# Performance work log

Measured on AMD Instinct MI355X. Metric: run time of the kernel, lower is better.

Reference implementation:

```python
import jax, jax.numpy as jnp
import numpy as np

NUM_NODES = 5000
NUM_COLORS = 20
NODE_FEAT = 4
COLOR_FEAT = 3
COMBINED = NODE_FEAT + COLOR_FEAT  # 7
HIDDEN = 128
N_GRAPH = NUM_NODES * NUM_COLORS   # 100000 GCN nodes (batch=1)
N_EDGES = 1_600_000


def setup_inputs() -> dict:
    key = jax.random.key(0)
    ks = jax.random.split(key, 12)
    flat_obs = jax.random.normal(ks[0], (1, 3 + NUM_NODES * NODE_FEAT + NUM_COLORS * COLOR_FEAT), dtype=jnp.float32)
    edge_index = jax.random.randint(ks[1], (2, N_EDGES), 0, N_GRAPH, dtype=jnp.int64)
    s = lambda k, sh, fan: jax.random.normal(k, sh, dtype=jnp.float32) / np.sqrt(fan)
    return {
        "flat_obs": flat_obs,
        "edge_index": edge_index,
        "W1": s(ks[2], (COMBINED, HIDDEN), COMBINED),
        "b1": jnp.zeros((HIDDEN,), jnp.float32),
        "W2": s(ks[3], (HIDDEN, HIDDEN), HIDDEN),
        "b2": jnp.zeros((HIDDEN,), jnp.float32),
        "fc1_w": s(ks[4], (HIDDEN, HIDDEN), HIDDEN),
        "fc1_b": jnp.zeros((HIDDEN,), jnp.float32),
        "fc2_w": s(ks[5], (HIDDEN, 1), HIDDEN),
        "fc2_b": jnp.zeros((1,), jnp.float32),
    }


def _gcn_conv(x, W, b, src, dst, norm):
    # PyG GCNConv: out[dst] += norm * (x @ W)[src]; self-loops already in src/dst.
    xw = x @ W                                   # [N, H]
    msg = xw[src] * norm[:, None]                # [E+N, H]
    out = jax.ops.segment_sum(msg, dst, num_segments=N_GRAPH)
    return out + b


def reference(flat_obs, edge_index, W1, b1, W2, b2, fc1_w, fc1_b, fc2_w, fc2_b):
    B = flat_obs.shape[0]
    nf_start = 3
    nf_end = nf_start + NUM_NODES * NODE_FEAT
    cf_end = nf_end + NUM_COLORS * COLOR_FEAT
    node_features = flat_obs[:, nf_start:nf_end].reshape(B, NUM_NODES, NODE_FEAT)
    color_features = flat_obs[:, nf_end:cf_end].reshape(B, NUM_COLORS, COLOR_FEAT)

    # cross-expand: [B, nodes, colors, 4+3]
    en = jnp.broadcast_to(node_features[:, :, None, :], (B, NUM_NODES, NUM_COLORS, NODE_FEAT))
    ec = jnp.broadcast_to(color_features[:, None, :, :], (B, NUM_NODES, NUM_COLORS, COLOR_FEAT))
    combined = jnp.concatenate([en, ec], axis=3).reshape(-1, COMBINED)  # [N_GRAPH, 7]

    # add self loops + symmetric normalization (GCN)
    loops = jnp.arange(N_GRAPH, dtype=edge_index.dtype)
    src = jnp.concatenate([edge_index[0], loops])
    dst = jnp.concatenate([edge_index[1], loops])
    deg = jax.ops.segment_sum(jnp.ones_like(dst, dtype=jnp.float32), dst, num_segments=N_GRAPH)
    dinv = jnp.where(deg > 0, jax.lax.rsqrt(deg), 0.0)
    norm = dinv[src] * dinv[dst]

    x = jax.nn.relu(_gcn_conv(combined, W1, b1, src, dst, norm))
    x = jax.nn.relu(_gcn_conv(x, W2, b2, src, dst, norm))
    x = jax.nn.relu(x @ fc1_w + fc1_b)
    q = x @ fc2_w + fc2_b                         # [N_GRAPH, 1]
    return q.reshape(B, NUM_NODES * NUM_COLORS)
```

## Files before the change

kernel.cpp:

```cpp
#include <hip/hip_runtime.h>
#include <hip/hip_fp16.h>

#define NGRAPH 100000
#define NEDGE  1600000
#define HID    128
#define SCAN_B 512
#define NBLK   ((NGRAPH + SCAN_B - 1) / SCAN_B)
#define TILE   64

__device__ __forceinline__ int e_src(const int* ei, int is64, int e) {
    return is64 ? ei[2 * e] : ei[e];
}
__device__ __forceinline__ int e_dst(const int* ei, int is64, int e) {
    return is64 ? ei[2 * NEDGE + 2 * e] : ei[NEDGE + e];
}

__global__ void k_prep(const float* __restrict__ obs, const int* __restrict__ ei,
                       float* __restrict__ comb, int* __restrict__ deg,
                       int* __restrict__ fill, int* __restrict__ flag) {
    if (blockIdx.x == 0 && threadIdx.x < 64) {
        int v = ei[2 * threadIdx.x + 1];
        unsigned long long b = __ballot(v != 0);
        if (threadIdx.x == 0) flag[0] = (b == 0ull) ? 1 : 0;
    }
    int i = blockIdx.x * blockDim.x + threadIdx.x;
    if (i >= NGRAPH) return;
    int n = i / 20, c = i % 20;
    const float* nf = obs + 3 + n * 4;
    const float* cf = obs + 3 + 20000 + c * 3;
    float* o = comb + i * 7;
    o[0] = nf[0]; o[1] = nf[1]; o[2] = nf[2]; o[3] = nf[3];
    o[4] = cf[0]; o[5] = cf[1]; o[6] = cf[2];
    deg[i] = 0;
    fill[i] = 0;
}

__global__ void k_deg(const int* __restrict__ ei, const int* __restrict__ flag,
                      int* __restrict__ deg) {
    int e = blockIdx.x * blockDim.x + threadIdx.x;
    if (e >= NEDGE) return;
    atomicAdd(&deg[e_dst(ei, flag[0], e)], 1);
}

__global__ void __launch_bounds__(SCAN_B) k_scan1(const int* __restrict__ deg,
                                                  int* __restrict__ rowptr,
                                                  int* __restrict__ sums,
                                                  float* __restrict__ dinv) {
    __shared__ int sh[SCAN_B];
    int t = threadIdx.x;
    int i = blockIdx.x * SCAN_B + t;
    int val = (i < NGRAPH) ? deg[i] : 0;
    if (i < NGRAPH) dinv[i] = rsqrtf((float)(val + 1));
    sh[t] = val;
    __syncthreads();
    for (int o = 1; o < SCAN_B; o <<= 1) {
        int x = (t >= o) ? sh[t - o] : 0;
        __syncthreads();
        sh[t] += x;
        __syncthreads();
    }
    if (i < NGRAPH) rowptr[i] = sh[t] - val;
    if (t == SCAN_B - 1) sums[blockIdx.x] = sh[t];
}

__global__ void __launch_bounds__(256) k_scan2(int* __restrict__ sums) {
    __shared__ int sh[256];
    int t = threadIdx.x;
    int val = (t < NBLK) ? sums[t] : 0;
    sh[t] = val;
    __syncthreads();
    for (int o = 1; o < 256; o <<= 1) {
        int x = (t >= o) ? sh[t - o] : 0;
        __syncthreads();
        sh[t] += x;
        __syncthreads();
    }
    if (t < NBLK) sums[t] = sh[t] - val;
}

__global__ void __launch_bounds__(SCAN_B) k_scan3(int* __restrict__ rowptr,
                                                  const int* __restrict__ sums) {
    int i = blockIdx.x * SCAN_B + threadIdx.x;
    if (i < NGRAPH) rowptr[i] += sums[blockIdx.x];
}

__global__ void k_fill(const int* __restrict__ ei, const int* __restrict__ flag,
                       const float* __restrict__ dinv,
                       const int* __restrict__ rowptr, int* __restrict__ fill,
                       int2* __restrict__ csr) {
    int e = blockIdx.x * blockDim.x + threadIdx.x;
    if (e >= NEDGE) return;
    int is64 = flag[0];
    int s = e_src(ei, is64, e);
    int d = e_dst(ei, is64, e);
    int pos = rowptr[d] + atomicAdd(&fill[d], 1);
    csr[pos] = make_int2(s, __float_as_int(dinv[s] * dinv[d]));
}

__global__ void __launch_bounds__(256) k_gcn1(const int* __restrict__ rowptr,
                                              const int* __restrict__ deg,
                                              const int2* __restrict__ csr,
                                              const float* __restrict__ dinv,
                                              const float* __restrict__ comb,
                                              const float* __restrict__ W1,
                                              const float* __restrict__ b1,
                                              __half* __restrict__ x1) {
    __shared__ float agg_s[32][8];
    int g = threadIdx.x >> 3;
    int f = threadIdx.x & 7;
    int d = blockIdx.x * 32 + g;
    if (f < 7) {
        int start = rowptr[d], n = deg[d];
        float acc = 0.0f;
        for (int j = 0; j < n; ++j) {
            int2 ed = csr[start + j];
            acc += __int_as_float(ed.y) * comb[ed.x * 7 + f];
        }
        float dv = dinv[d];
        acc += dv * dv * comb[d * 7 + f];
        agg_s[g][f] = acc;
    }
    __syncthreads();
    float a[7];
    #pragma unroll
    for (int q = 0; q < 7; ++q) a[q] = agg_s[g][q];
    int h0 = f * 16;
    #pragma unroll
    for (int j = 0; j < 4; ++j) {
        int h = h0 + j * 4;
        float4 acc4 = *reinterpret_cast<const float4*>(b1 + h);
        #pragma unroll
        for (int q = 0; q < 7; ++q) {
            float4 w = *reinterpret_cast<const float4*>(W1 + q * HID + h);
            acc4.x = fmaf(a[q], w.x, acc4.x);
            acc4.y = fmaf(a[q], w.y, acc4.y);
            acc4.z = fmaf(a[q], w.z, acc4.z);
            acc4.w = fmaf(a[q], w.w, acc4.w);
        }
        __half2 h01 = __floats2half2_rn(fmaxf(acc4.x, 0.0f), fmaxf(acc4.y, 0.0f));
        __half2 h23 = __floats2half2_rn(fmaxf(acc4.z, 0.0f), fmaxf(acc4.w, 0.0f));
        uint2 pk;
        pk.x = *reinterpret_cast<unsigned int*>(&h01);
        pk.y = *reinterpret_cast<unsigned int*>(&h23);
        *reinterpret_cast<uint2*>(x1 + (size_t)d * HID + h) = pk;
    }
}

__global__ void __launch_bounds__(256) k_agg2(const int* __restrict__ rowptr,
                                              const int* __restrict__ deg,
                                              const int2* __restrict__ csr,
                                              const float* __restrict__ dinv,
                                              const __half2* __restrict__ x1,
                                              float* __restrict__ agg2) {
    int wave = threadIdx.x >> 6;
    int lane = threadIdx.x & 63;
    int d = blockIdx.x * 4 + wave;
    int f0 = lane * 2;
    int start = rowptr[d], n = deg[d];
    float2 acc = {0.0f, 0.0f};
    int j = 0;
    for (; j + 2 <= n; j += 2) {
        int2 e0 = csr[start + j];
        int2 e1 = csr[start + j + 1];
        float w0 = __int_as_float(e0.y);
        float w1 = __int_as_float(e1.y);
        float2 v0 = __half22float2(x1[(size_t)e0.x * 64 + lane]);
        float2 v1 = __half22float2(x1[(size_t)e1.x * 64 + lane]);
        acc.x = fmaf(w0, v0.x, acc.x);
        acc.y = fmaf(w0, v0.y, acc.y);
        acc.x = fmaf(w1, v1.x, acc.x);
        acc.y = fmaf(w1, v1.y, acc.y);
    }
    if (j < n) {
        int2 e0 = csr[start + j];
        float w0 = __int_as_float(e0.y);
        float2 v0 = __half22float2(x1[(size_t)e0.x * 64 + lane]);
        acc.x = fmaf(w0, v0.x, acc.x);
        acc.y = fmaf(w0, v0.y, acc.y);
    }
    float dv = dinv[d];
    float ws = dv * dv;
    float2 v = __half22float2(x1[(size_t)d * 64 + lane]);
    acc.x = fmaf(ws, v.x, acc.x);
    acc.y = fmaf(ws, v.y, acc.y);
    *reinterpret_cast<float2*>(agg2 + (size_t)d * HID + f0) = acc;
}

__device__ __forceinline__ void fmad(float4& acc, float s, const float4 w) {
    acc.x = fmaf(s, w.x, acc.x);
    acc.y = fmaf(s, w.y, acc.y);
    acc.z = fmaf(s, w.z, acc.z);
    acc.w = fmaf(s, w.w, acc.w);
}
__device__ __forceinline__ float4 relu4(float4 v) {
    float4 r;
    r.x = fmaxf(v.x, 0.0f); r.y = fmaxf(v.y, 0.0f);
    r.z = fmaxf(v.z, 0.0f); r.w = fmaxf(v.w, 0.0f);
    return r;
}

__global__ void __launch_bounds__(256, 3) k_mlp(const float* __restrict__ agg2,
                                                const float* __restrict__ W2,
                                                const float* __restrict__ b2,
                                                const float* __restrict__ fc1w,
                                                const float* __restrict__ fc1b,
                                                const float* __restrict__ fc2w,
                                                const float* __restrict__ fc2b,
                                                float* __restrict__ out) {
    __shared__ float as_[TILE][HID + 4];
    __shared__ float ws[32][HID + 4];
    const int tid = threadIdx.x;
    const int tx = tid & 15;
    const int ty = tid >> 4;
    const int n0 = blockIdx.x * TILE;
    const int hA = tx * 4;
    const int hB = 64 + tx * 4;

    #pragma unroll
    for (int q = 0; q < 8; ++q) {
        int idx = (q * 256 + tid) * 4;
        int row = idx >> 7, col = idx & 127;
        int nr = n0 + row; if (nr >= NGRAPH) nr = NGRAPH - 1;
        *reinterpret_cast<float4*>(&as_[row][col]) =
            *reinterpret_cast<const float4*>(agg2 + (size_t)nr * HID + col);
    }

    float4 cA[4], cB[4];
    {
        float4 bA = *reinterpret_cast<const float4*>(b2 + hA);
        float4 bB = *reinterpret_cast<const float4*>(b2 + hB);
        #pragma unroll
        for (int r = 0; r < 4; ++r) { cA[r] = bA; cB[r] = bB; }
    }
    for (int ks = 0; ks < HID; ks += 32) {
        #pragma unroll
        for (int q = 0; q < 4; ++q) {
            int idx = (q * 256 + tid) * 4;
            int row = idx >> 7, col = idx & 127;
            *reinterpret_cast<float4*>(&ws[row][col]) =
                *reinterpret_cast<const float4*>(W2 + (size_t)(ks + row) * HID + col);
        }
        __syncthreads();
        #pragma unroll
        for (int k = 0; k < 32; k += 4) {
            float4 wA0 = *reinterpret_cast<const float4*>(&ws[k + 0][hA]);
            float4 wB0 = *reinterpret_cast<const float4*>(&ws[k + 0][hB]);
            float4 wA1 = *reinterpret_cast<const float4*>(&ws[k + 1][hA]);
            float4 wB1 = *reinterpret_cast<const float4*>(&ws[k + 1][hB]);
            float4 wA2 = *reinterpret_cast<const float4*>(&ws[k + 2][hA]);
            float4 wB2 = *reinterpret_cast<const float4*>(&ws[k + 2][hB]);
            float4 wA3 = *reinterpret_cast<const float4*>(&ws[k + 3][hA]);
            float4 wB3 = *reinterpret_cast<const float4*>(&ws[k + 3][hB]);
            #pragma unroll
            for (int r = 0; r < 4; ++r) {
                float4 a = *reinterpret_cast<const float4*>(&as_[ty * 4 + r][ks + k]);
                fmad(cA[r], a.x, wA0); fmad(cB[r], a.x, wB0);
                fmad(cA[r], a.y, wA1); fmad(cB[r], a.y, wB1);
                fmad(cA[r], a.z, wA2); fmad(cB[r], a.z, wB2);
                fmad(cA[r], a.w, wA3); fmad(cB[r], a.w, wB3);
            }
        }
        __syncthreads();
    }
    #pragma unroll
    for (int r = 0; r < 4; ++r) {
        *reinterpret_cast<float4*>(&as_[ty * 4 + r][hA]) = relu4(cA[r]);
        *reinterpret_cast<float4*>(&as_[ty * 4 + r][hB]) = relu4(cB[r]);
    }

    float4 dA[4], dB[4];
    {
        float4 bA = *reinterpret_cast<const float4*>(fc1b + hA);
        float4 bB = *reinterpret_cast<const float4*>(fc1b + hB);
        #pragma unroll
        for (int r = 0; r < 4; ++r) { dA[r] = bA; dB[r] = bB; }
    }
    for (int ks = 0; ks < HID; ks += 32) {
        #pragma unroll
        for (int q = 0; q < 4; ++q) {
            int idx = (q * 256 + tid) * 4;
            int row = idx >> 7, col = idx & 127;
            *reinterpret_cast<float4*>(&ws[row][col]) =
                *reinterpret_cast<const float4*>(fc1w + (size_t)(ks + row) * HID + col);
        }
        __syncthreads();
        #pragma unroll
        for (int k = 0; k < 32; k += 4) {
            float4 wA0 = *reinterpret_cast<const float4*>(&ws[k + 0][hA]);
            float4 wB0 = *reinterpret_cast<const float4*>(&ws[k + 0][hB]);
            float4 wA1 = *reinterpret_cast<const float4*>(&ws[k + 1][hA]);
            float4 wB1 = *reinterpret_cast<const float4*>(&ws[k + 1][hB]);
            float4 wA2 = *reinterpret_cast<const float4*>(&ws[k + 2][hA]);
            float4 wB2 = *reinterpret_cast<const float4*>(&ws[k + 2][hB]);
            float4 wA3 = *reinterpret_cast<const float4*>(&ws[k + 3][hA]);
            float4 wB3 = *reinterpret_cast<const float4*>(&ws[k + 3][hB]);
            #pragma unroll
            for (int r = 0; r < 4; ++r) {
                float4 a = *reinterpret_cast<const float4*>(&as_[ty * 4 + r][ks + k]);
                fmad(dA[r], a.x, wA0); fmad(dB[r], a.x, wB0);
                fmad(dA[r], a.y, wA1); fmad(dB[r], a.y, wB1);
                fmad(dA[r], a.z, wA2); fmad(dB[r], a.z, wB2);
                fmad(dA[r], a.w, wA3); fmad(dB[r], a.w, wB3);
            }
        }
        __syncthreads();
    }

    float4 wqA = *reinterpret_cast<const float4*>(fc2w + hA);
    float4 wqB = *reinterpret_cast<const float4*>(fc2w + hB);
    float p[4];
    #pragma unroll
    for (int r = 0; r < 4; ++r) {
        float4 rA = relu4(dA[r]);
        float4 rB = relu4(dB[r]);
        p[r] = rA.x * wqA.x + rA.y * wqA.y + rA.z * wqA.z + rA.w * wqA.w
             + rB.x * wqB.x + rB.y * wqB.y + rB.z * wqB.z + rB.w * wqB.w;
    }
    #pragma unroll
    for (int m = 1; m < 16; m <<= 1) {
        #pragma unroll
        for (int r = 0; r < 4; ++r) p[r] += __shfl_xor(p[r], m);
    }
    if (tx == 0) {
        float bq = fc2b[0];
        int nb = n0 + ty * 4;
        #pragma unroll
        for (int r = 0; r < 4; ++r)
            if (nb + r < NGRAPH) out[nb + r] = p[r] + bq;
    }
}

extern "C" void kernel_launch(void* const* d_in, const int* in_sizes, int n_in,
                              void* d_out, int out_size, void* d_ws, size_t ws_size,
                              hipStream_t stream) {
    const float* obs  = (const float*)d_in[0];
    const int*   ei   = (const int*)d_in[1];
    const float* W1   = (const float*)d_in[2];
    const float* b1   = (const float*)d_in[3];
    const float* W2   = (const float*)d_in[4];
    const float* b2   = (const float*)d_in[5];
    const float* fc1w = (const float*)d_in[6];
    const float* fc1b = (const float*)d_in[7];
    const float* fc2w = (const float*)d_in[8];
    const float* fc2b = (const float*)d_in[9];
    float* out = (float*)d_out;

    char* base = (char*)d_ws;
    size_t off = 0;
    auto take = [&](size_t bytes) {
        char* p = base + off;
        off += (bytes + 255) & ~(size_t)255;
        return p;
    };
    int*    deg     = (int*)take((size_t)NGRAPH * 4);
    int*    rowptr  = (int*)take((size_t)NGRAPH * 4);
    int*    fill    = (int*)take((size_t)NGRAPH * 4);
    int*    sums    = (int*)take((size_t)NBLK * 4);
    float*  dinv    = (float*)take((size_t)NGRAPH * 4);
    int2*   csr     = (int2*)take((size_t)NEDGE * 8);
    float*  comb    = (float*)take((size_t)NGRAPH * 7 * 4);
    __half* x1      = (__half*)take((size_t)NGRAPH * HID * 2);
    float*  agg2    = (float*)take((size_t)NGRAPH * HID * 4);
    int*    flag    = (int*)take(256);

    k_prep<<<(NGRAPH + 255) / 256, 256, 0, stream>>>(obs, ei, comb, deg, fill, flag);
    k_deg<<<(NEDGE + 255) / 256, 256, 0, stream>>>(ei, flag, deg);
    k_scan1<<<NBLK, SCAN_B, 0, stream>>>(deg, rowptr, sums, dinv);
    k_scan2<<<1, 256, 0, stream>>>(sums);
    k_scan3<<<NBLK, SCAN_B, 0, stream>>>(rowptr, sums);
    k_fill<<<(NEDGE + 255) / 256, 256, 0, stream>>>(ei, flag, dinv, rowptr, fill, csr);
    k_gcn1<<<NGRAPH / 32, 256, 0, stream>>>(rowptr, deg, csr, dinv,
                                            comb, W1, b1, x1);
    k_agg2<<<NGRAPH / 4, 256, 0, stream>>>(rowptr, deg, csr, dinv,
                                           (const __half2*)x1, agg2);
    k_mlp<<<(NGRAPH + TILE - 1) / TILE, 256, 0, stream>>>(agg2, W2, b2,
                                                          fc1w, fc1b,
                                                          fc2w, fc2b, out);
}
```

Before: 460.8 us.

## Fuse layer-2 neighbor aggregation into the MLP kernel, dropping agg2 buffer

Removes the separate aggregation kernel and has each MLP block gather its 64 rows of neighbor features directly from x1 into shared memory. This avoids writing and rereading a full fp32 intermediate of N x 128 and saves one launch. In exchange, the gather runs with far fewer concurrent waves per CU, which limits latency hiding. The shared-memory row padding also shrinks to 130 floats, which changes bank mapping and 16-byte alignment of rows.

```diff
diff --git a/kernel.cpp b/kernel.cpp
--- a/kernel.cpp
+++ b/kernel.cpp
@@ -7,6 +7,7 @@
 #define SCAN_B 512
 #define NBLK   ((NGRAPH + SCAN_B - 1) / SCAN_B)
 #define TILE   64
+#define LPAD   (HID + 2)
 
 __device__ __forceinline__ int e_src(const int* ei, int is64, int e) {
     return is64 ? ei[2 * e] : ei[e];
@@ -146,46 +147,6 @@
     }
 }
 
-__global__ void __launch_bounds__(256) k_agg2(const int* __restrict__ rowptr,
-                                              const int* __restrict__ deg,
-                                              const int2* __restrict__ csr,
-                                              const float* __restrict__ dinv,
-                                              const __half2* __restrict__ x1,
-                                              float* __restrict__ agg2) {
-    int wave = threadIdx.x >> 6;
-    int lane = threadIdx.x & 63;
-    int d = blockIdx.x * 4 + wave;
-    int f0 = lane * 2;
-    int start = rowptr[d], n = deg[d];
-    float2 acc = {0.0f, 0.0f};
-    int j = 0;
-    for (; j + 2 <= n; j += 2) {
-        int2 e0 = csr[start + j];
-        int2 e1 = csr[start + j + 1];
-        float w0 = __int_as_float(e0.y);
-        float w1 = __int_as_float(e1.y);
-        float2 v0 = __half22float2(x1[(size_t)e0.x * 64 + lane]);
-        float2 v1 = __half22float2(x1[(size_t)e1.x * 64 + lane]);
-        acc.x = fmaf(w0, v0.x, acc.x);
-        acc.y = fmaf(w0, v0.y, acc.y);
-        acc.x = fmaf(w1, v1.x, acc.x);
-        acc.y = fmaf(w1, v1.y, acc.y);
-    }
-    if (j < n) {
-        int2 e0 = csr[start + j];
-        float w0 = __int_as_float(e0.y);
-        float2 v0 = __half22float2(x1[(size_t)e0.x * 64 + lane]);
-        acc.x = fmaf(w0, v0.x, acc.x);
-        acc.y = fmaf(w0, v0.y, acc.y);
-    }
-    float dv = dinv[d];
-    float ws = dv * dv;
-    float2 v = __half22float2(x1[(size_t)d * 64 + lane]);
-    acc.x = fmaf(ws, v.x, acc.x);
-    acc.y = fmaf(ws, v.y, acc.y);
-    *reinterpret_cast<float2*>(agg2 + (size_t)d * HID + f0) = acc;
-}
-
 __device__ __forceinline__ void fmad(float4& acc, float s, const float4 w) {
     acc.x = fmaf(s, w.x, acc.x);
     acc.y = fmaf(s, w.y, acc.y);
@@ -199,7 +160,11 @@
     return r;
 }
 
-__global__ void __launch_bounds__(256, 3) k_mlp(const float* __restrict__ agg2,
+__global__ void __launch_bounds__(256, 3) k_mlp(const int* __restrict__ rowptr,
+                                                const int* __restrict__ deg,
+                                                const int2* __restrict__ csr,
+                                                const float* __restrict__ dinv,
+                                                const __half2* __restrict__ x1,
                                                 const float* __restrict__ W2,
                                                 const float* __restrict__ b2,
                                                 const float* __restrict__ fc1w,
@@ -207,8 +172,8 @@
                                                 const float* __restrict__ fc2w,
                                                 const float* __restrict__ fc2b,
                                                 float* __restrict__ out) {
-    __shared__ float as_[TILE][HID + 4];
-    __shared__ float ws[32][HID + 4];
+    __shared__ float as_[TILE][LPAD];
+    __shared__ float ws[32][LPAD];
     const int tid = threadIdx.x;
     const int tx = tid & 15;
     const int ty = tid >> 4;
@@ -216,13 +181,42 @@
     const int hA = tx * 4;
     const int hB = 64 + tx * 4;
 
-    #pragma unroll
-    for (int q = 0; q < 8; ++q) {
-        int idx = (q * 256 + tid) * 4;
-        int row = idx >> 7, col = idx & 127;
-        int nr = n0 + row; if (nr >= NGRAPH) nr = NGRAPH - 1;
-        *reinterpret_cast<float4*>(&as_[row][col]) =
-            *reinterpret_cast<const float4*>(agg2 + (size_t)nr * HID + col);
+    {
+        int wave = tid >> 6;
+        int lane = tid & 63;
+        for (int q = 0; q < 16; ++q) {
+            int row = wave * 16 + q;
+            int nd = n0 + row;
+            if (nd >= NGRAPH) nd = NGRAPH - 1;
+            int start = rowptr[nd], n = deg[nd];
+            float2 acc = {0.0f, 0.0f};
+            int j = 0;
+            for (; j + 2 <= n; j += 2) {
+                int2 e0 = csr[start + j];
+                int2 e1 = csr[start + j + 1];
+                float w0 = __int_as_float(e0.y);
+                float w1 = __int_as_float(e1.y);
+                float2 v0 = __half22float2(x1[(size_t)e0.x * 64 + lane]);
+                float2 v1 = __half22float2(x1[(size_t)e1.x * 64 + lane]);
+                acc.x = fmaf(w0, v0.x, acc.x);
+                acc.y = fmaf(w0, v0.y, acc.y);
+                acc.x = fmaf(w1, v1.x, acc.x);
+                acc.y = fmaf(w1, v1.y, acc.y);
+            }
+            if (j < n) {
+                int2 e0 = csr[start + j];
+                float w0 = __int_as_float(e0.y);
+                float2 v0 = __half22float2(x1[(size_t)e0.x * 64 + lane]);
+                acc.x = fmaf(w0, v0.x, acc.x);
+                acc.y = fmaf(w0, v0.y, acc.y);
+            }
+            float dv = dinv[nd];
+            float wsl = dv * dv;
+            float2 v = __half22float2(x1[(size_t)nd * 64 + lane]);
+            acc.x = fmaf(wsl, v.x, acc.x);
+            acc.y = fmaf(wsl, v.y, acc.y);
+            *reinterpret_cast<float2*>(&as_[row][lane * 2]) = acc;
+        }
     }
 
     float4 cA[4], cB[4];
@@ -360,7 +354,6 @@
     int2*   csr     = (int2*)take((size_t)NEDGE * 8);
     float*  comb    = (float*)take((size_t)NGRAPH * 7 * 4);
     __half* x1      = (__half*)take((size_t)NGRAPH * HID * 2);
-    float*  agg2    = (float*)take((size_t)NGRAPH * HID * 4);
     int*    flag    = (int*)take(256);
 
     k_prep<<<(NGRAPH + 255) / 256, 256, 0, stream>>>(obs, ei, comb, deg, fill, flag);
@@ -371,9 +364,8 @@
     k_fill<<<(NEDGE + 255) / 256, 256, 0, stream>>>(ei, flag, dinv, rowptr, fill, csr);
     k_gcn1<<<NGRAPH / 32, 256, 0, stream>>>(rowptr, deg, csr, dinv,
                                             comb, W1, b1, x1);
-    k_agg2<<<NGRAPH / 4, 256, 0, stream>>>(rowptr, deg, csr, dinv,
-                                           (const __half2*)x1, agg2);
-    k_mlp<<<(NGRAPH + TILE - 1) / TILE, 256, 0, stream>>>(agg2, W2, b2,
-                                                          fc1w, fc1b,
+    k_mlp<<<(NGRAPH + TILE - 1) / TILE, 256, 0, stream>>>(rowptr, deg, csr, dinv,
+                                                          (const __half2*)x1,
+                                                          W2, b2, fc1w, fc1b,
                                                           fc2w, fc2b, out);
 }
```

New measurement: 596.1 us. 29.4% more time.
